# Performance work log

Hardware: AMD Instinct MI355X
Metric: run time of the kernel (lower is better)

The kernel has to match this reference:

```python
import jax, jax.numpy as jnp
import numpy as np

D_IN = 1024
D_OUT = 1024
SEQ = 2048
BATCH = 4


def setup_inputs() -> dict:
    key = jax.random.key(0)
    ks = jax.random.split(key, 7)
    s_in = 1.0 / np.sqrt(D_IN)
    return {
        "x": jax.random.normal(ks[0], (BATCH, SEQ, D_IN), dtype=jnp.float32),
        "Wq": jax.random.normal(ks[1], (D_IN, D_OUT), dtype=jnp.float32) * s_in,
        "bq": jax.random.normal(ks[2], (D_OUT,), dtype=jnp.float32) * 0.01,
        "Wk": jax.random.normal(ks[3], (D_IN, D_OUT), dtype=jnp.float32) * s_in,
        "bk": jax.random.normal(ks[4], (D_OUT,), dtype=jnp.float32) * 0.01,
        "Wv": jax.random.normal(ks[5], (D_IN, D_OUT), dtype=jnp.float32) * s_in,
        "bv": jax.random.normal(ks[6], (D_OUT,), dtype=jnp.float32) * 0.01,
    }


def reference(x, Wq, bq, Wk, bk, Wv, bv):
    # x: [b, n, d_in]
    b, n, d_in = x.shape
    q = x @ Wq + bq  # [b, n, d_out]
    k = x @ Wk + bk
    v = x @ Wv + bv
    scale = 1.0 / jnp.sqrt(jnp.asarray(d_in, x.dtype))
    scores = jnp.einsum("bqd,bkd->bqk", q, k) * scale  # [b, n, n]
    causal = jnp.triu(jnp.ones((n, n), dtype=bool), k=1)  # True above diagonal
    scores = jnp.where(causal, -jnp.inf, scores)
    weights = jax.nn.softmax(scores, axis=-1)
    # dropout p=0.0 -> identity
    context = jnp.einsum("bqk,bkd->bqd", weights, v)
    return context
```

## Files before the change

kernel.cpp:

```cpp
#include <hip/hip_runtime.h>

typedef unsigned short u16;
typedef __bf16 bf16x8 __attribute__((ext_vector_type(8)));
typedef float floatx4 __attribute__((ext_vector_type(4)));

#define B_ 4
#define SEQ 2048
#define DIM 1024

__device__ __forceinline__ u16 f2bf(float f) {
    unsigned u = __builtin_bit_cast(unsigned, f);
    u += 0x7FFFu + ((u >> 16) & 1u);
    return (u16)(u >> 16);
}
__device__ __forceinline__ float bf2f(u16 h) {
    unsigned u = ((unsigned)h) << 16;
    return __builtin_bit_cast(float, u);
}

#define GPTR(p) ((const __attribute__((address_space(1))) void*)(p))
#define LPTR(p) ((__attribute__((address_space(3))) void*)(p))
#define GLD(src, dstp) __builtin_amdgcn_global_load_lds(GPTR(src), LPTR(dstp), 16, 0, 0)

__global__ __launch_bounds__(256) void convert_x(const float4* __restrict__ x,
                                                 ushort4* __restrict__ xb) {
    int i = blockIdx.x * 256 + threadIdx.x;
    float4 v = x[i];
    ushort4 o;
    o.x = f2bf(v.x); o.y = f2bf(v.y); o.z = f2bf(v.z); o.w = f2bf(v.w);
    xb[i] = o;
}

__global__ __launch_bounds__(256) void transpose_w(const float* __restrict__ Wq,
                                                   const float* __restrict__ Wk,
                                                   const float* __restrict__ Wv,
                                                   u16* __restrict__ Wt) {
    __shared__ u16 t[64][66];
    const int z = blockIdx.z;
    const float* W = (z == 0) ? Wq : ((z == 1) ? Wk : Wv);
    u16* out = Wt + (size_t)z * DIM * DIM;
    const int tx = threadIdx.x, ty = threadIdx.y;
    const int k0 = blockIdx.x * 64, n0 = blockIdx.y * 64;
#pragma unroll
    for (int j = 0; j < 8; j++) {
        int k = ty + 8 * j;
        float2 v = *(const float2*)(W + (size_t)(k0 + k) * DIM + n0 + 2 * tx);
        t[2 * tx][k] = f2bf(v.x);
        t[2 * tx + 1][k] = f2bf(v.y);
    }
    __syncthreads();
#pragma unroll
    for (int j = 0; j < 8; j++) {
        int n = ty + 8 * j;
        ushort2 o;
        o.x = t[n][2 * tx];
        o.y = t[n][2 * tx + 1];
        *(ushort2*)(out + (size_t)(n0 + n) * DIM + k0 + 2 * tx) = o;
    }
}

__device__ __forceinline__ void mainloop(
    const u16* __restrict__ Ab, const u16* __restrict__ Bb, int lda, int ldb,
    int Kt, u16* lsA, u16* lsB, int tid, int wave, int quad, int l15,
    int wm, int wn, floatx4 (&acc)[4][4]) {
    const int srow = tid >> 2;
    const int scol = ((tid & 3) ^ ((tid >> 3) & 3)) * 8;
    const u16* gA = Ab + (size_t)srow * lda + scol;
    const u16* gB = Bb + (size_t)srow * ldb + scol;
    const int swq = (quad ^ ((l15 >> 1) & 3)) * 8;

#pragma unroll
    for (int i = 0; i < 4; i++)
#pragma unroll
        for (int j = 0; j < 4; j++) {
            floatx4 zz = {0.f, 0.f, 0.f, 0.f};
            acc[i][j] = zz;
        }

    for (int k0 = 0; k0 < Kt; k0 += 64) {
#pragma unroll
        for (int h = 0; h < 2; h++)
#pragma unroll
            for (int c = 0; c < 2; c++) {
                __builtin_amdgcn_global_load_lds(
                    GPTR(gA + (size_t)c * 64 * lda + h * 32),
                    LPTR(lsA + h * 4096 + c * 2048 + wave * 512), 16, 0, 0);
                __builtin_amdgcn_global_load_lds(
                    GPTR(gB + (size_t)c * 64 * ldb + h * 32),
                    LPTR(lsB + h * 4096 + c * 2048 + wave * 512), 16, 0, 0);
            }
        gA += 64; gB += 64;
        __syncthreads();

#pragma unroll
        for (int h = 0; h < 2; h++) {
            bf16x8 af[4];
#pragma unroll
            for (int i = 0; i < 4; i++)
                af[i] = *(const bf16x8*)(lsA + h * 4096 + (wm + i * 16 + l15) * 32 + swq);
#pragma unroll
            for (int j = 0; j < 4; j++) {
                bf16x8 bfr = *(const bf16x8*)(lsB + h * 4096 + (wn + j * 16 + l15) * 32 + swq);
#pragma unroll
                for (int i = 0; i < 4; i++)
                    acc[i][j] = __builtin_amdgcn_mfma_f32_16x16x32_bf16(af[i], bfr, acc[i][j], 0, 0, 0);
            }
        }
        __syncthreads();
    }
}

__global__ __launch_bounds__(512, 2) void gemm_qkv_r3(
    const u16* __restrict__ A, const u16* __restrict__ Bt, u16* __restrict__ QK,
    const float* __restrict__ b0, const float* __restrict__ b1,
    const float* __restrict__ b2, u16* __restrict__ VtOut) {
    __shared__ union {
        u16 stage[3][24576];
        u16 T[256 * 128];
    } sm;

    const int tid = threadIdx.x;
    const int wave = tid >> 6, lane = tid & 63;
    const int quad = lane >> 4, l15 = lane & 15;
    const int wm = (wave >> 2) * 64;
    const int wn = (wave & 3) * 64;
    const int wl = wave * 512;

    const int bid = blockIdx.x;
    const int wgid = (bid & 7) * 96 + (bid >> 3);
    const int mt = wgid & 63, nt = wgid >> 6;

    const int srow = tid >> 3;
    const int sseg = (tid & 7) ^ (srow & 7);
    const u16* gA = A + (size_t)(mt * 128 + srow) * DIM + sseg * 8;
    const u16* gB = Bt + (size_t)(nt * 256 + srow) * DIM + sseg * 8;

    u16* p0 = &sm.stage[0][0];
    u16* p1 = &sm.stage[1][0];
    u16* p2 = &sm.stage[2][0];

    const int s0 = (quad ^ (l15 & 7)) * 8;
    const int rAoff = (wm + l15) * 64;
    const int rBoff = 8192 + (wn + l15) * 64;

    floatx4 acc[4][4];
#pragma unroll
    for (int i = 0; i < 4; i++)
#pragma unroll
        for (int j = 0; j < 4; j++) {
            floatx4 zz = {0.f, 0.f, 0.f, 0.f};
            acc[i][j] = zz;
        }

#define QKV_STAGE(bW) do { \
    GLD(gA,                      (bW) + wl); \
    GLD(gA + (size_t)64 * DIM,   (bW) + 4096 + wl); \
    GLD(gB,                      (bW) + 8192 + wl); \
    GLD(gB + (size_t)64 * DIM,   (bW) + 12288 + wl); \
    GLD(gB + (size_t)128 * DIM,  (bW) + 16384 + wl); \
    GLD(gB + (size_t)192 * DIM,  (bW) + 20480 + wl); \
    gA += 64; gB += 64; } while (0)

#define QKV_TILE(bR, bW, STG, EVM) do { \
    __builtin_amdgcn_s_barrier(); \
    if (STG) QKV_STAGE(bW); \
    const u16* rA_ = (bR) + rAoff; \
    const u16* rB_ = (bR) + rBoff; \
    bf16x8 a_[4], bv_[4]; \
    _Pragma("unroll") for (int i_ = 0; i_ < 4; ++i_) a_[i_] = *(const bf16x8*)(rA_ + i_ * 1024 + s0); \
    _Pragma("unroll") for (int j_ = 0; j_ < 4; ++j_) bv_[j_] = *(const bf16x8*)(rB_ + j_ * 1024 + s0); \
    __builtin_amdgcn_s_setprio(1); \
    _Pragma("unroll") for (int j_ = 0; j_ < 4; ++j_) \
    _Pragma("unroll") for (int i_ = 0; i_ < 4; ++i_) \
        acc[i_][j_] = __builtin_amdgcn_mfma_f32_16x16x32_bf16(a_[i_], bv_[j_], acc[i_][j_], 0, 0, 0); \
    __builtin_amdgcn_s_setprio(0); \
    _Pragma("unroll") for (int i_ = 0; i_ < 4; ++i_) a_[i_] = *(const bf16x8*)(rA_ + i_ * 1024 + (s0 ^ 32)); \
    _Pragma("unroll") for (int j_ = 0; j_ < 4; ++j_) bv_[j_] = *(const bf16x8*)(rB_ + j_ * 1024 + (s0 ^ 32)); \
    __builtin_amdgcn_s_setprio(1); \
    _Pragma("unroll") for (int j_ = 0; j_ < 4; ++j_) \
    _Pragma("unroll") for (int i_ = 0; i_ < 4; ++i_) \
        acc[i_][j_] = __builtin_amdgcn_mfma_f32_16x16x32_bf16(a_[i_], bv_[j_], acc[i_][j_], 0, 0, 0); \
    __builtin_amdgcn_s_setprio(0); \
    if ((EVM) == 6) { asm volatile("s_waitcnt vmcnt(6)" ::: "memory"); } \
    else if ((EVM) == 0) { asm volatile("s_waitcnt vmcnt(0)" ::: "memory"); } \
    } while (0)

    QKV_STAGE(p0);
    QKV_STAGE(p1);
    asm volatile("s_waitcnt vmcnt(6)" ::: "memory");

    for (int tt = 0; tt < 4; ++tt) {
        QKV_TILE(p0, p2, 1, 6);
        QKV_TILE(p1, p0, 1, 6);
        QKV_TILE(p2, p1, 1, 6);
    }
    QKV_TILE(p0, p2, 1, 6);
    QKV_TILE(p1, p0, 1, 6);
    QKV_TILE(p2, p1, 0, 0);
    QKV_TILE(p0, p1, 0, -1);

#undef QKV_TILE
#undef QKV_STAGE

    const int z = nt >> 2;
    const int nc = (nt & 3) * 256 + wn + l15;
    const float* bias = (z == 0) ? b0 : ((z == 1) ? b1 : b2);

    if (z < 2) {
        u16* Cb = QK + (size_t)z * B_ * SEQ * DIM;
        const int m00 = mt * 128 + wm + quad * 4;
#pragma unroll
        for (int j = 0; j < 4; ++j) {
            float bv2 = bias[nc + j * 16];
#pragma unroll
            for (int i = 0; i < 4; ++i)
#pragma unroll
                for (int r = 0; r < 4; ++r)
                    Cb[(size_t)(m00 + i * 16 + r) * DIM + nc + j * 16] =
                        f2bf(acc[i][j][r] + bv2);
        }
        return;
    }

    float addj[4];
#pragma unroll
    for (int j = 0; j < 4; ++j) addj[j] = bias[nc + j * 16];
    __syncthreads();
#pragma unroll
    for (int i = 0; i < 4; ++i) {
        const int tb = wm + i * 16 + quad * 4;
#pragma unroll
        for (int j = 0; j < 4; ++j) {
            const int d = wn + j * 16 + l15;
            ushort4 o;
            o.x = f2bf(acc[i][j][0] + addj[j]);
            o.y = f2bf(acc[i][j][1] + addj[j]);
            o.z = f2bf(acc[i][j][2] + addj[j]);
            o.w = f2bf(acc[i][j][3] + addj[j]);
            *(ushort4*)&sm.T[d * 128 + (tb ^ ((d & 7) << 3))] = o;
        }
    }
    __syncthreads();
    const int bI = mt >> 4;
    const int sbase = (mt & 15) * 128;
    u16* Vb = VtOut + (size_t)bI * DIM * SEQ + (size_t)(nt - 8) * 256 * SEQ + sbase;
#pragma unroll
    for (int k = 0; k < 8; ++k) {
        int idx = tid + 512 * k;
        int d = idx >> 4, sg = idx & 15;
        uint4 v = *(const uint4*)&sm.T[d * 128 + ((sg * 8) ^ ((d & 7) << 3))];
        *(uint4*)(Vb + (size_t)d * SEQ + sg * 8) = v;
    }
}

__global__ __launch_bounds__(256, 3) void gemm_scores(
    const u16* __restrict__ Q, const u16* __restrict__ K, u16* __restrict__ S,
    float scale) {
    const int j = blockIdx.x;
    int ym = (int)((sqrtf(8.f * (float)j + 1.f) - 1.f) * 0.5f);
    while ((ym + 1) * (ym + 2) / 2 <= j) ++ym;
    while (ym * (ym + 1) / 2 > j) --ym;
    const int xn = j - ym * (ym + 1) / 2;

    __shared__ u16 lsA[128 * 64];
    __shared__ u16 lsB[128 * 64];
    const int tid = threadIdx.x;
    const int wave = tid >> 6, lane = tid & 63;
    const int quad = lane >> 4, l15 = lane & 15;
    const int wm = (wave >> 1) * 64, wn = (wave & 1) * 64;
    const int z = blockIdx.z;

    const u16* Ab = Q + (size_t)z * SEQ * DIM + (size_t)ym * 128 * DIM;
    const u16* Bb = K + (size_t)z * SEQ * DIM + (size_t)xn * 128 * DIM;
    floatx4 acc[4][4];
    mainloop(Ab, Bb, DIM, DIM, DIM, lsA, lsB,
             tid, wave, quad, l15, wm, wn, acc);

    u16* Cb = S + (size_t)z * SEQ * SEQ;
    const int m0 = ym * 128 + wm + quad * 4;
    const int n0 = xn * 128 + wn + l15;
#pragma unroll
    for (int jj = 0; jj < 4; jj++)
#pragma unroll
        for (int i = 0; i < 4; i++)
#pragma unroll
            for (int r = 0; r < 4; r++)
                Cb[(size_t)(m0 + i * 16 + r) * SEQ + (n0 + jj * 16)] = f2bf(acc[i][jj][r] * scale);
}

__global__ __launch_bounds__(256, 3) void gemm_pv(
    const u16* __restrict__ P, const u16* __restrict__ Vt, float* __restrict__ O) {
    const int ym = (blockIdx.z & 2) ? (int)blockIdx.y : (15 - (int)blockIdx.y);
    __shared__ u16 lsA[128 * 64];
    __shared__ u16 lsB[128 * 64];
    const int tid = threadIdx.x;
    const int wave = tid >> 6, lane = tid & 63;
    const int quad = lane >> 4, l15 = lane & 15;
    const int wm = (wave >> 1) * 64, wn = (wave & 1) * 64;
    const int z = blockIdx.z;

    const u16* Ab = P + (size_t)z * SEQ * SEQ + (size_t)ym * 128 * SEQ;
    const u16* Bb = Vt + (size_t)z * DIM * SEQ + (size_t)blockIdx.x * 128 * SEQ;
    const int Kt = (ym + 1) * 128;
    floatx4 acc[4][4];
    mainloop(Ab, Bb, SEQ, SEQ, Kt, lsA, lsB,
             tid, wave, quad, l15, wm, wn, acc);

    float* Cf = O + (size_t)z * SEQ * DIM;
    const int m0 = ym * 128 + wm + quad * 4;
    const int n0 = blockIdx.x * 128 + wn + l15;
#pragma unroll
    for (int j = 0; j < 4; j++)
#pragma unroll
        for (int i = 0; i < 4; i++)
#pragma unroll
            for (int r = 0; r < 4; r++)
                Cf[(size_t)(m0 + i * 16 + r) * DIM + (n0 + j * 16)] = acc[i][j][r];
}

__global__ __launch_bounds__(256) void softmax_causal(u16* __restrict__ S) {
    const int q = blockIdx.x, b = blockIdx.y, tid = threadIdx.x;
    u16* row = S + ((size_t)b * SEQ + q) * SEQ;
    const int L = q + 1;
    const int Z = ((q >> 7) + 1) << 7;
    const int k0 = tid * 8;
    __shared__ float redm[4], reds[4];

    uint4 rv = ((const uint4*)row)[tid];
    unsigned w[4] = {rv.x, rv.y, rv.z, rv.w};
    float f[8];
#pragma unroll
    for (int e = 0; e < 8; e++) {
        u16 h = (u16)((w[e >> 1] >> ((e & 1) * 16)) & 0xFFFFu);
        f[e] = (k0 + e < L) ? bf2f(h) : -3.0e38f;
    }
    float m = f[0];
#pragma unroll
    for (int e = 1; e < 8; e++) m = fmaxf(m, f[e]);
#pragma unroll
    for (int o = 32; o > 0; o >>= 1) m = fmaxf(m, __shfl_xor(m, o));
    if ((tid & 63) == 0) redm[tid >> 6] = m;
    __syncthreads();
    m = fmaxf(fmaxf(redm[0], redm[1]), fmaxf(redm[2], redm[3]));

    float p[8];
    float s = 0.f;
#pragma unroll
    for (int e = 0; e < 8; e++) {
        p[e] = (k0 + e < L) ? __expf(f[e] - m) : 0.f;
        s += p[e];
    }
#pragma unroll
    for (int o = 32; o > 0; o >>= 1) s += __shfl_xor(s, o);
    if ((tid & 63) == 0) reds[tid >> 6] = s;
    __syncthreads();
    s = reds[0] + reds[1] + reds[2] + reds[3];
    const float inv = 1.0f / s;

    if (k0 < Z) {
        unsigned o2[4];
#pragma unroll
        for (int e = 0; e < 4; e++) {
            unsigned lo = f2bf(p[2 * e] * inv);
            unsigned hi = f2bf(p[2 * e + 1] * inv);
            o2[e] = lo | (hi << 16);
        }
        uint4 ov = {o2[0], o2[1], o2[2], o2[3]};
        ((uint4*)row)[tid] = ov;
    }
}

extern "C" void kernel_launch(void* const* d_in, const int* in_sizes, int n_in,
                              void* d_out, int out_size, void* d_ws, size_t ws_size,
                              hipStream_t stream) {
    const float* x = (const float*)d_in[0];
    const float* Wq = (const float*)d_in[1];
    const float* bq = (const float*)d_in[2];
    const float* Wk = (const float*)d_in[3];
    const float* bk = (const float*)d_in[4];
    const float* Wv = (const float*)d_in[5];
    const float* bv = (const float*)d_in[6];
    float* out = (float*)d_out;

    char* ws = (char*)d_ws;
    const size_t MB = 1024ull * 1024ull;
    u16* S = (u16*)ws;
    u16* xb = (u16*)ws;
    u16* Wt = (u16*)(ws + 16 * MB);
    u16* QK = (u16*)(ws + 32 * MB);
    u16* Vt = (u16*)(ws + 64 * MB);
    const size_t MAT = (size_t)B_ * SEQ * DIM;
    u16* Q = QK;
    u16* Km = QK + MAT;

    const float scale = 0.03125f;

    convert_x<<<8192, 256, 0, stream>>>((const float4*)x, (ushort4*)xb);
    transpose_w<<<dim3(16, 16, 3), dim3(32, 8), 0, stream>>>(Wq, Wk, Wv, Wt);
    gemm_qkv_r3<<<dim3(768), dim3(512), 0, stream>>>(xb, Wt, QK, bq, bk, bv, Vt);
    gemm_scores<<<dim3(136, 1, 4), 256, 0, stream>>>(Q, Km, S, scale);
    softmax_causal<<<dim3(SEQ, B_), 256, 0, stream>>>(S);
    gemm_pv<<<dim3(8, 16, 4), 256, 0, stream>>>(S, Vt, out);
}
```

Baseline: 254.3 us.

## Fuse causal softmax into scores GEMM via row-block counters; merge prep kernels

The separate softmax kernel is removed. Each scores GEMM block writes its tile, then increments a per-(batch, row-block) atomic counter and spins until every tile in that row block is done. The blocks sharing a row block then split its 128 rows between them and run the softmax in place, with one wave per row. This drops a launch and lets the softmax read recently written data, likely still in cache. The x conversion and weight transpose are also merged into one launch. The cost is an inter-block spin wait, which relies on all 544 scores blocks being co-resident and needs a counter memset.

```diff
diff --git a/kernel.cpp b/kernel.cpp
--- a/kernel.cpp
+++ b/kernel.cpp
@@ -22,25 +22,26 @@
 #define LPTR(p) ((__attribute__((address_space(3))) void*)(p))
 #define GLD(src, dstp) __builtin_amdgcn_global_load_lds(GPTR(src), LPTR(dstp), 16, 0, 0)
 
-__global__ __launch_bounds__(256) void convert_x(const float4* __restrict__ x,
-                                                 ushort4* __restrict__ xb) {
-    int i = blockIdx.x * 256 + threadIdx.x;
-    float4 v = x[i];
-    ushort4 o;
-    o.x = f2bf(v.x); o.y = f2bf(v.y); o.z = f2bf(v.z); o.w = f2bf(v.w);
-    xb[i] = o;
-}
-
-__global__ __launch_bounds__(256) void transpose_w(const float* __restrict__ Wq,
-                                                   const float* __restrict__ Wk,
-                                                   const float* __restrict__ Wv,
-                                                   u16* __restrict__ Wt) {
+__global__ __launch_bounds__(256) void prep(
+    const float4* __restrict__ x, ushort4* __restrict__ xb,
+    const float* __restrict__ Wq, const float* __restrict__ Wk,
+    const float* __restrict__ Wv, u16* __restrict__ Wt) {
+    const int bx = blockIdx.x, tid = threadIdx.x;
+    if (bx < 8192) {
+        int i = bx * 256 + tid;
+        float4 v = x[i];
+        ushort4 o;
+        o.x = f2bf(v.x); o.y = f2bf(v.y); o.z = f2bf(v.z); o.w = f2bf(v.w);
+        xb[i] = o;
+        return;
+    }
     __shared__ u16 t[64][66];
-    const int z = blockIdx.z;
+    const int b = bx - 8192;
+    const int kx = b & 15, ny = (b >> 4) & 15, z = b >> 8;
     const float* W = (z == 0) ? Wq : ((z == 1) ? Wk : Wv);
     u16* out = Wt + (size_t)z * DIM * DIM;
-    const int tx = threadIdx.x, ty = threadIdx.y;
-    const int k0 = blockIdx.x * 64, n0 = blockIdx.y * 64;
+    const int tx = tid & 31, ty = tid >> 5;
+    const int k0 = kx * 64, n0 = ny * 64;
 #pragma unroll
     for (int j = 0; j < 8; j++) {
         int k = ty + 8 * j;
@@ -253,9 +254,9 @@
     }
 }
 
-__global__ __launch_bounds__(256, 3) void gemm_scores(
+__global__ __launch_bounds__(256, 3) void scores_sm(
     const u16* __restrict__ Q, const u16* __restrict__ K, u16* __restrict__ S,
-    float scale) {
+    float scale, int* __restrict__ cnt) {
     const int j = blockIdx.x;
     int ym = (int)((sqrtf(8.f * (float)j + 1.f) - 1.f) * 0.5f);
     while ((ym + 1) * (ym + 2) / 2 <= j) ++ym;
@@ -276,7 +277,7 @@
     mainloop(Ab, Bb, DIM, DIM, DIM, lsA, lsB,
              tid, wave, quad, l15, wm, wn, acc);
 
-    u16* Cb = S + (size_t)z * SEQ * SEQ;
+    u16* Sz = S + (size_t)z * SEQ * SEQ;
     const int m0 = ym * 128 + wm + quad * 4;
     const int n0 = xn * 128 + wn + l15;
 #pragma unroll
@@ -285,7 +286,76 @@
         for (int i = 0; i < 4; i++)
 #pragma unroll
             for (int r = 0; r < 4; r++)
-                Cb[(size_t)(m0 + i * 16 + r) * SEQ + (n0 + jj * 16)] = f2bf(acc[i][jj][r] * scale);
+                Sz[(size_t)(m0 + i * 16 + r) * SEQ + (n0 + jj * 16)] = f2bf(acc[i][jj][r] * scale);
+
+    __threadfence();
+    __syncthreads();
+    const int ci = z * 16 + ym;
+    if (tid == 0) {
+        __hip_atomic_fetch_add(&cnt[ci], 1, __ATOMIC_RELEASE, __HIP_MEMORY_SCOPE_AGENT);
+        while (__hip_atomic_load(&cnt[ci], __ATOMIC_ACQUIRE, __HIP_MEMORY_SCOPE_AGENT) < ym + 1)
+            __builtin_amdgcn_s_sleep(2);
+    }
+    __syncthreads();
+    __threadfence();
+
+    const int Zs = (ym + 1) * 128;
+    const int period = ym + 1;
+    u16* Srow0 = Sz + (size_t)ym * 128 * SEQ;
+    const int c0 = lane * 8;
+    for (int t = wave; ; t += 4) {
+        const int r = xn + t * period;
+        if (r >= 128) break;
+        const int L = ym * 128 + r + 1;
+        u16* prow = Srow0 + (size_t)r * SEQ;
+        float f[4][8];
+        bool act[4];
+        float mx = -3.0e38f;
+#pragma unroll
+        for (int u = 0; u < 4; ++u) {
+            const int cb = c0 + 512 * u;
+            act[u] = cb < Zs;
+            if (act[u]) {
+                uint4 rv = *(const uint4*)(prow + cb);
+                unsigned wv[4] = {rv.x, rv.y, rv.z, rv.w};
+#pragma unroll
+                for (int e = 0; e < 8; ++e) {
+                    u16 h = (u16)((wv[e >> 1] >> ((e & 1) * 16)) & 0xFFFFu);
+                    f[u][e] = (cb + e < L) ? bf2f(h) : -3.0e38f;
+                    mx = fmaxf(mx, f[u][e]);
+                }
+            }
+        }
+#pragma unroll
+        for (int o = 32; o > 0; o >>= 1) mx = fmaxf(mx, __shfl_xor(mx, o));
+        float s = 0.f;
+#pragma unroll
+        for (int u = 0; u < 4; ++u)
+            if (act[u]) {
+#pragma unroll
+                for (int e = 0; e < 8; ++e) {
+                    float pe = (f[u][e] > -1.0e38f) ? __expf(f[u][e] - mx) : 0.f;
+                    f[u][e] = pe;
+                    s += pe;
+                }
+            }
+#pragma unroll
+        for (int o = 32; o > 0; o >>= 1) s += __shfl_xor(s, o);
+        const float inv = 1.0f / s;
+#pragma unroll
+        for (int u = 0; u < 4; ++u)
+            if (act[u]) {
+                unsigned o2[4];
+#pragma unroll
+                for (int e = 0; e < 4; ++e) {
+                    unsigned lo = f2bf(f[u][2 * e] * inv);
+                    unsigned hi = f2bf(f[u][2 * e + 1] * inv);
+                    o2[e] = lo | (hi << 16);
+                }
+                uint4 ov = {o2[0], o2[1], o2[2], o2[3]};
+                *(uint4*)(prow + c0 + 512 * u) = ov;
+            }
+    }
 }
 
 __global__ __launch_bounds__(256, 3) void gemm_pv(
@@ -316,58 +386,6 @@
 #pragma unroll
             for (int r = 0; r < 4; r++)
                 Cf[(size_t)(m0 + i * 16 + r) * DIM + (n0 + j * 16)] = acc[i][j][r];
-}
-
-__global__ __launch_bounds__(256) void softmax_causal(u16* __restrict__ S) {
-    const int q = blockIdx.x, b = blockIdx.y, tid = threadIdx.x;
-    u16* row = S + ((size_t)b * SEQ + q) * SEQ;
-    const int L = q + 1;
-    const int Z = ((q >> 7) + 1) << 7;
-    const int k0 = tid * 8;
-    __shared__ float redm[4], reds[4];
-
-    uint4 rv = ((const uint4*)row)[tid];
-    unsigned w[4] = {rv.x, rv.y, rv.z, rv.w};
-    float f[8];
-#pragma unroll
-    for (int e = 0; e < 8; e++) {
-        u16 h = (u16)((w[e >> 1] >> ((e & 1) * 16)) & 0xFFFFu);
-        f[e] = (k0 + e < L) ? bf2f(h) : -3.0e38f;
-    }
-    float m = f[0];
-#pragma unroll
-    for (int e = 1; e < 8; e++) m = fmaxf(m, f[e]);
-#pragma unroll
-    for (int o = 32; o > 0; o >>= 1) m = fmaxf(m, __shfl_xor(m, o));
-    if ((tid & 63) == 0) redm[tid >> 6] = m;
-    __syncthreads();
-    m = fmaxf(fmaxf(redm[0], redm[1]), fmaxf(redm[2], redm[3]));
-
-    float p[8];
-    float s = 0.f;
-#pragma unroll
-    for (int e = 0; e < 8; e++) {
-        p[e] = (k0 + e < L) ? __expf(f[e] - m) : 0.f;
-        s += p[e];
-    }
-#pragma unroll
-    for (int o = 32; o > 0; o >>= 1) s += __shfl_xor(s, o);
-    if ((tid & 63) == 0) reds[tid >> 6] = s;
-    __syncthreads();
-    s = reds[0] + reds[1] + reds[2] + reds[3];
-    const float inv = 1.0f / s;
-
-    if (k0 < Z) {
-        unsigned o2[4];
-#pragma unroll
-        for (int e = 0; e < 4; e++) {
-            unsigned lo = f2bf(p[2 * e] * inv);
-            unsigned hi = f2bf(p[2 * e + 1] * inv);
-            o2[e] = lo | (hi << 16);
-        }
-        uint4 ov = {o2[0], o2[1], o2[2], o2[3]};
-        ((uint4*)row)[tid] = ov;
-    }
 }
 
 extern "C" void kernel_launch(void* const* d_in, const int* in_sizes, int n_in,
@@ -389,16 +407,16 @@
     u16* Wt = (u16*)(ws + 16 * MB);
     u16* QK = (u16*)(ws + 32 * MB);
     u16* Vt = (u16*)(ws + 64 * MB);
+    int* cnt = (int*)(ws + 2048);
     const size_t MAT = (size_t)B_ * SEQ * DIM;
     u16* Q = QK;
     u16* Km = QK + MAT;
 
     const float scale = 0.03125f;
 
-    convert_x<<<8192, 256, 0, stream>>>((const float4*)x, (ushort4*)xb);
-    transpose_w<<<dim3(16, 16, 3), dim3(32, 8), 0, stream>>>(Wq, Wk, Wv, Wt);
+    prep<<<8960, 256, 0, stream>>>((const float4*)x, (ushort4*)xb, Wq, Wk, Wv, Wt);
     gemm_qkv_r3<<<dim3(768), dim3(512), 0, stream>>>(xb, Wt, QK, bq, bk, bv, Vt);
-    gemm_scores<<<dim3(136, 1, 4), 256, 0, stream>>>(Q, Km, S, scale);
-    softmax_causal<<<dim3(SEQ, B_), 256, 0, stream>>>(S);
+    hipMemsetAsync(cnt, 0, 256, stream);
+    scores_sm<<<dim3(136, 1, 4), 256, 0, stream>>>(Q, Km, S, scale, cnt);
     gemm_pv<<<dim3(8, 16, 4), 256, 0, stream>>>(S, Vt, out);
 }
```

New measurement: 434.8 us. 1.71x slower.
